# Performance work log

Hardware: AMD Instinct MI355X
Metric: run time of the kernel (lower is better)

The kernel has to match this reference:

```python
import jax, jax.numpy as jnp
import numpy as np

L, B, T, D, H, M = 2, 4, 1024, 256, 4, 1024
EPS = 1e-5  # hk.LayerNorm default


def setup_inputs() -> dict:
    key = jax.random.key(0)
    ks = jax.random.split(key, 12)
    s_in = (2.0 / D) ** 0.5       # VarianceScaling(2.0), fan_in = D
    s_o = (2.0 / (H * D)) ** 0.5  # fan_in = H*D for final projection
    s_m = (1.0 / M) ** 0.5
    g = lambda k, shape, s: jax.random.normal(k, shape, jnp.float32) * s
    return {
        "queries": g(ks[0], (B, T, D), 1.0),
        "Wq": g(ks[1], (L, D, H * D), s_in),
        "bq": jnp.zeros((L, H * D), jnp.float32),
        "Wk": g(ks[2], (L, D, H * D), s_in),
        "bk": jnp.zeros((L, H * D), jnp.float32),
        "Wv": g(ks[3], (L, D, H * D), s_in),
        "bv": jnp.zeros((L, H * D), jnp.float32),
        "Wo": g(ks[4], (L, H * D, D), s_o),
        "bo": jnp.zeros((L, D), jnp.float32),
        "ln1_s": jnp.ones((L, D), jnp.float32),
        "ln1_b": jnp.zeros((L, D), jnp.float32),
        "W1": g(ks[5], (L, D, M), s_in),
        "b1": jnp.zeros((L, M), jnp.float32),
        "W2": g(ks[6], (L, M, D), s_m),
        "b2": jnp.zeros((L, D), jnp.float32),
        "ln2_s": jnp.ones((L, D), jnp.float32),
        "ln2_b": jnp.zeros((L, D), jnp.float32),
    }


def _layernorm(x, s, o):
    m = jnp.mean(x, axis=-1, keepdims=True)
    v = jnp.var(x, axis=-1, keepdims=True)
    return (x - m) * jax.lax.rsqrt(v + EPS) * s + o


def _block(x, Wq, bq, Wk, bk, Wv, bv, Wo, bo, ln1_s, ln1_b, W1, b1, W2, b2, ln2_s, ln2_b):
    # Multi-head self-attention with per-head dim = D (key_size == qkv_size)
    q = (x @ Wq + bq).reshape(B, T, H, D)
    k = (x @ Wk + bk).reshape(B, T, H, D)
    v = (x @ Wv + bv).reshape(B, T, H, D)
    q = q / jnp.sqrt(jnp.float32(D))
    attn = jnp.einsum('bqhd,bkhd->bhqk', q, k)   # [B,H,T,T]
    attn = jax.nn.softmax(attn, axis=-1)
    o = jnp.einsum('bhqk,bkhd->bqhd', attn, v).reshape(B, T, H * D)
    o = o @ Wo + bo
    # post-norm residual 1
    x = _layernorm(o + x, ln1_s, ln1_b)
    # MLP: Linear(D->M) + ReLU + Linear(M->D)
    h = jax.nn.relu(x @ W1 + b1)
    m = h @ W2 + b2
    return _layernorm(m + x, ln2_s, ln2_b)


def reference(queries, Wq, bq, Wk, bk, Wv, bv, Wo, bo, ln1_s, ln1_b,
              W1, b1, W2, b2, ln2_s, ln2_b):
    x = queries
    for i in range(L):
        x = _block(x, Wq[i], bq[i], Wk[i], bk[i], Wv[i], bv[i], Wo[i], bo[i],
                   ln1_s[i], ln1_b[i], W1[i], b1[i], W2[i], b2[i],
                   ln2_s[i], ln2_b[i])
    return x
```

## Files before the change

### kernel.cpp

```cpp
#include <hip/hip_runtime.h>
#include <hip/hip_bf16.h>

#define CL 2
#define CB 4
#define CT 1024
#define CD 256
#define CH 4
#define CM 1024
#define CHD (CH * CD)
#define NROW (CB * CT)

typedef unsigned short ushort_t;
typedef __attribute__((ext_vector_type(8))) short short8v;
typedef __attribute__((ext_vector_type(4))) float float4v;

#define LOG2E 1.44269504088896f

__device__ __forceinline__ float bf2f(unsigned short u) {
    return __uint_as_float(((unsigned int)u) << 16);
}
__device__ __forceinline__ unsigned short f2bf(float f) {
    unsigned int x = __float_as_uint(f);
    return (unsigned short)((x + 0x7fffu + ((x >> 16) & 1u)) >> 16);
}

__global__ __launch_bounds__(256) void detect_kernel(
    const ushort_t* __restrict__ w, int n, int* __restrict__ flag)
{
    __shared__ int red[256];
    int c = 0;
    for (int i = threadIdx.x; i < n; i += 256) {
        float v = bf2f(w[i]);
        if (!(fabsf(v) <= 1e6f)) c++;
    }
    red[threadIdx.x] = c;
    __syncthreads();
    for (int s = 128; s > 0; s >>= 1) {
        if (threadIdx.x < s) red[threadIdx.x] += red[threadIdx.x + s];
        __syncthreads();
    }
    if (threadIdx.x == 0) flag[0] = (red[0] < 8) ? 1 : 0;
}

__global__ __launch_bounds__(256) void tconv_kernel(
    const void* __restrict__ in, ushort_t* __restrict__ out,
    int R, int C, long inzs, long outzs, long ioff,
    const int* __restrict__ flagp)
{
    const int fbf = *flagp;
    __shared__ float tile[32][33];
    const long zi = ioff + (long)blockIdx.z * inzs;
    const long zo = (long)blockIdx.z * outzs;
    const int r0 = blockIdx.y * 32;
    const int c0 = blockIdx.x * 32;
    const int tx = threadIdx.x & 31;
    const int ty = threadIdx.x >> 5;
#pragma unroll
    for (int i = 0; i < 32; i += 8) {
        const long idx = zi + (long)(r0 + ty + i) * C + c0 + tx;
        tile[ty + i][tx] = fbf ? bf2f(((const ushort_t*)in)[idx])
                               : ((const float*)in)[idx];
    }
    __syncthreads();
#pragma unroll
    for (int i = 0; i < 32; i += 8)
        out[zo + (long)(c0 + ty + i) * R + r0 + tx] = f2bf(tile[tx][ty + i]);
}

__global__ __launch_bounds__(256) void qkv_proj(
    const ushort_t* __restrict__ A, const ushort_t* __restrict__ B,
    const void* __restrict__ bq, const void* __restrict__ bk,
    const void* __restrict__ bv, ushort_t* __restrict__ qk,
    ushort_t* __restrict__ vT, long boff, const int* __restrict__ flagp)
{
    const long m0 = (long)blockIdx.y * 128;
    const long n0 = (long)blockIdx.x * 128;

    __shared__ __align__(16) ushort_t As[128 * 32];
    __shared__ __align__(16) ushort_t Bs[128 * 32];

    const int tid = threadIdx.x;
    const int wave = tid >> 6;
    const int lane = tid & 63;
    const int quad = lane >> 4;
    const int lrow = lane & 15;
    const int wm = (wave >> 1) * 64;
    const int wn = (wave & 1) * 64;

    float4v acc[4][4];
#pragma unroll
    for (int i = 0; i < 4; ++i)
#pragma unroll
        for (int j = 0; j < 4; ++j)
            acc[i][j] = (float4v){0.f, 0.f, 0.f, 0.f};

    for (int k0 = 0; k0 < 256; k0 += 32) {
        __syncthreads();
#pragma unroll
        for (int p = 0; p < 2; ++p) {
            const int c = p * 256 + tid;
            const int row = c >> 2;
            const int kk = (c & 3) << 3;
            *reinterpret_cast<short8v*>(&As[c << 3]) =
                *reinterpret_cast<const short8v*>(&A[(m0 + row) * 256 + k0 + kk]);
            *reinterpret_cast<short8v*>(&Bs[c << 3]) =
                *reinterpret_cast<const short8v*>(&B[(n0 + row) * 256 + k0 + kk]);
        }
        __syncthreads();

        short8v af[4], bfv[4];
#pragma unroll
        for (int i = 0; i < 4; ++i) {
            af[i]  = *reinterpret_cast<const short8v*>(&As[(wm + i * 16 + lrow) * 32 + quad * 8]);
            bfv[i] = *reinterpret_cast<const short8v*>(&Bs[(wn + i * 16 + lrow) * 32 + quad * 8]);
        }
#pragma unroll
        for (int mi = 0; mi < 4; ++mi)
#pragma unroll
            for (int ni = 0; ni < 4; ++ni)
                acc[mi][ni] = __builtin_amdgcn_mfma_f32_16x16x32_bf16(
                    af[mi], bfv[ni], acc[mi][ni], 0, 0, 0);
    }

    const int fbf = *flagp;
#pragma unroll
    for (int mi = 0; mi < 4; ++mi) {
#pragma unroll
        for (int ni = 0; ni < 4; ++ni) {
            const long col = n0 + wn + ni * 16 + lrow;
            const long row0 = m0 + wm + mi * 16 + quad * 4;
            const void* bp;
            long bn;
            if (col < 1024)      { bp = bq; bn = col; }
            else if (col < 2048) { bp = bk; bn = col - 1024; }
            else                 { bp = bv; bn = col - 2048; }
            const float bias = fbf ? bf2f(((const ushort_t*)bp)[boff + bn])
                                   : ((const float*)bp)[boff + bn];
            if (col < 2048) {
#pragma unroll
                for (int r = 0; r < 4; ++r)
                    qk[(row0 + r) * 2048 + col] = f2bf(acc[mi][ni][r] + bias);
            } else {
                const long d = col - 2048;
                const long addr = ((row0 >> 10) << 2) * 262144 + d * 1024 + (row0 & 1023);
                ushort4 u;
                u.x = f2bf(acc[mi][ni][0] + bias);
                u.y = f2bf(acc[mi][ni][1] + bias);
                u.z = f2bf(acc[mi][ni][2] + bias);
                u.w = f2bf(acc[mi][ni][3] + bias);
                *reinterpret_cast<ushort4*>(&vT[addr]) = u;
            }
        }
    }
}

template <int AMODE>
__global__ __launch_bounds__(256) void mgemm64s(
    const ushort_t* __restrict__ A, const ushort_t* __restrict__ Ap1,
    const float2* __restrict__ ml, const ushort_t* __restrict__ B,
    float* __restrict__ P, int K2, int lda, int ldb)
{
    const int z = blockIdx.z;
    const long m0 = (long)blockIdx.y * 64;
    const long n0 = (long)blockIdx.x * 64;
    const int k_beg = z * K2;

    __shared__ __align__(16) ushort_t As[64 * 32];
    __shared__ __align__(16) ushort_t Bs[64 * 32];

    const int tid = threadIdx.x;
    const int wave = tid >> 6;
    const int lane = tid & 63;
    const int quad = lane >> 4;
    const int lrow = lane & 15;
    const int wm = (wave >> 1) * 32;
    const int wn = (wave & 1) * 32;

    const int ar = tid >> 2;
    const int ak = (tid & 3) << 3;

    float4v acc[2][2];
#pragma unroll
    for (int i = 0; i < 2; ++i)
#pragma unroll
        for (int j = 0; j < 2; ++j)
            acc[i][j] = (float4v){0.f, 0.f, 0.f, 0.f};

    for (int k0 = k_beg; k0 < k_beg + K2; k0 += 32) {
        __syncthreads();
        if constexpr (AMODE == 0) {
            *reinterpret_cast<short8v*>(&As[tid << 3]) =
                *reinterpret_cast<const short8v*>(&A[(m0 + ar) * (long)lda + k0 + ak]);
        } else {
            const long m = m0 + ar;
            const int hh = (k0 + ak) >> 8;
            const int bh = ((int)(m >> 10) << 2) + hh;
            const int trow = (int)(m & 1023);
            const float2 v0 = ml[bh * 1024 + trow];
            const float2 v1 = ml[(16 + bh) * 1024 + trow];
            const float mm = fmaxf(v0.x, v1.x);
            const float a0 = exp2f(v0.x - mm);
            const float a1 = exp2f(v1.x - mm);
            const float inv = 1.0f / (v0.y * a0 + v1.y * a1);
            const ushort4 u0a = *reinterpret_cast<const ushort4*>(&A[m * 1024 + k0 + ak]);
            const ushort4 u0b = *reinterpret_cast<const ushort4*>(&A[m * 1024 + k0 + ak + 4]);
            const ushort4 u1a = *reinterpret_cast<const ushort4*>(&Ap1[m * 1024 + k0 + ak]);
            const ushort4 u1b = *reinterpret_cast<const ushort4*>(&Ap1[m * 1024 + k0 + ak + 4]);
            short8v t8;
            t8[0] = (short)f2bf((bf2f(u0a.x) * a0 + bf2f(u1a.x) * a1) * inv);
            t8[1] = (short)f2bf((bf2f(u0a.y) * a0 + bf2f(u1a.y) * a1) * inv);
            t8[2] = (short)f2bf((bf2f(u0a.z) * a0 + bf2f(u1a.z) * a1) * inv);
            t8[3] = (short)f2bf((bf2f(u0a.w) * a0 + bf2f(u1a.w) * a1) * inv);
            t8[4] = (short)f2bf((bf2f(u0b.x) * a0 + bf2f(u1b.x) * a1) * inv);
            t8[5] = (short)f2bf((bf2f(u0b.y) * a0 + bf2f(u1b.y) * a1) * inv);
            t8[6] = (short)f2bf((bf2f(u0b.z) * a0 + bf2f(u1b.z) * a1) * inv);
            t8[7] = (short)f2bf((bf2f(u0b.w) * a0 + bf2f(u1b.w) * a1) * inv);
            *reinterpret_cast<short8v*>(&As[tid << 3]) = t8;
        }
        *reinterpret_cast<short8v*>(&Bs[tid << 3]) =
            *reinterpret_cast<const short8v*>(&B[(n0 + ar) * (long)ldb + k0 + ak]);
        __syncthreads();

        short8v af[2], bfv[2];
#pragma unroll
        for (int i = 0; i < 2; ++i) {
            af[i]  = *reinterpret_cast<const short8v*>(&As[(wm + i * 16 + lrow) * 32 + quad * 8]);
            bfv[i] = *reinterpret_cast<const short8v*>(&Bs[(wn + i * 16 + lrow) * 32 + quad * 8]);
        }
#pragma unroll
        for (int mi = 0; mi < 2; ++mi)
#pragma unroll
            for (int ni = 0; ni < 2; ++ni)
                acc[mi][ni] = __builtin_amdgcn_mfma_f32_16x16x32_bf16(
                    af[mi], bfv[ni], acc[mi][ni], 0, 0, 0);
    }

    float* Pz = P + (long)z * NROW * CD;
#pragma unroll
    for (int mi = 0; mi < 2; ++mi)
#pragma unroll
        for (int ni = 0; ni < 2; ++ni) {
            const long col = n0 + wn + ni * 16 + lrow;
            const long row0 = m0 + wm + mi * 16 + quad * 4;
#pragma unroll
            for (int r = 0; r < 4; ++r)
                Pz[(row0 + r) * CD + col] = acc[mi][ni][r];
        }
}

template <int RELU>
__global__ __launch_bounds__(256) void mgemm64b(
    const ushort_t* __restrict__ A, const ushort_t* __restrict__ B,
    const void* __restrict__ bias, ushort_t* __restrict__ C,
    int K, int lda, int ldb, int ldc, long boff,
    const int* __restrict__ flagp)
{
    const long m0 = (long)blockIdx.y * 64;
    const long n0 = (long)blockIdx.x * 64;

    __shared__ __align__(16) ushort_t As[64 * 32];
    __shared__ __align__(16) ushort_t Bs[64 * 32];

    const int tid = threadIdx.x;
    const int wave = tid >> 6;
    const int lane = tid & 63;
    const int quad = lane >> 4;
    const int lrow = lane & 15;
    const int wm = (wave >> 1) * 32;
    const int wn = (wave & 1) * 32;

    const int ar = tid >> 2;
    const int ak = (tid & 3) << 3;

    float4v acc[2][2];
#pragma unroll
    for (int i = 0; i < 2; ++i)
#pragma unroll
        for (int j = 0; j < 2; ++j)
            acc[i][j] = (float4v){0.f, 0.f, 0.f, 0.f};

    for (int k0 = 0; k0 < K; k0 += 32) {
        __syncthreads();
        *reinterpret_cast<short8v*>(&As[tid << 3]) =
            *reinterpret_cast<const short8v*>(&A[(m0 + ar) * (long)lda + k0 + ak]);
        *reinterpret_cast<short8v*>(&Bs[tid << 3]) =
            *reinterpret_cast<const short8v*>(&B[(n0 + ar) * (long)ldb + k0 + ak]);
        __syncthreads();

        short8v af[2], bfv[2];
#pragma unroll
        for (int i = 0; i < 2; ++i) {
            af[i]  = *reinterpret_cast<const short8v*>(&As[(wm + i * 16 + lrow) * 32 + quad * 8]);
            bfv[i] = *reinterpret_cast<const short8v*>(&Bs[(wn + i * 16 + lrow) * 32 + quad * 8]);
        }
#pragma unroll
        for (int mi = 0; mi < 2; ++mi)
#pragma unroll
            for (int ni = 0; ni < 2; ++ni)
                acc[mi][ni] = __builtin_amdgcn_mfma_f32_16x16x32_bf16(
                    af[mi], bfv[ni], acc[mi][ni], 0, 0, 0);
    }

    const int fbf = *flagp;
#pragma unroll
    for (int mi = 0; mi < 2; ++mi)
#pragma unroll
        for (int ni = 0; ni < 2; ++ni) {
            const long col = n0 + wn + ni * 16 + lrow;
            const long row0 = m0 + wm + mi * 16 + quad * 4;
            const float bv = fbf ? bf2f(((const ushort_t*)bias)[boff + col])
                                 : ((const float*)bias)[boff + col];
#pragma unroll
            for (int r = 0; r < 4; ++r) {
                float v = acc[mi][ni][r] + bv;
                if (RELU) v = fmaxf(v, 0.f);
                C[(row0 + r) * (long)ldc + col] = f2bf(v);
            }
        }
}

__global__ __launch_bounds__(256) void flash_attn(
    const ushort_t* __restrict__ qk, const ushort_t* __restrict__ vT,
    ushort_t* __restrict__ op0, ushort_t* __restrict__ op1,
    float2* __restrict__ ml)
{
    const int bx = blockIdx.x;
    const int bh = bx & 15;
    const int qt = (bx >> 4) & 15;
    const int ck = bx >> 8;
    const int b = bh >> 2, h = bh & 3;

    __shared__ __align__(16) ushort_t Ks[32 * 264];
    __shared__ __align__(16) ushort_t Vs[256 * 40];
    __shared__ __align__(16) ushort_t Ps[4][16 * 40];

    const int tid = threadIdx.x;
    const int wave = tid >> 6;
    const int lane = tid & 63;
    const int quad = lane >> 4;
    const int lrow = lane & 15;

    const long qrow0 = (long)b * CT + qt * 64;
    const int qcol = h * 256;
    const int kcol = 1024 + h * 256;
    const long vbase = (long)bh * 256 * 1024;
    const float SC = 0.0625f * LOG2E;

    short8v qf[8];
#pragma unroll
    for (int kk = 0; kk < 8; ++kk)
        qf[kk] = *reinterpret_cast<const short8v*>(
            &qk[(qrow0 + wave * 16 + lrow) * 2048 + qcol + kk * 32 + quad * 8]);

    float m4[4], l4[4];
#pragma unroll
    for (int r = 0; r < 4; ++r) { m4[r] = -1e30f; l4[r] = 0.f; }
    float4v oacc[16];
#pragma unroll
    for (int i = 0; i < 16; ++i) oacc[i] = (float4v){0.f, 0.f, 0.f, 0.f};

    const int t_beg = ck * 512;
    for (int t0 = t_beg; t0 < t_beg + 512; t0 += 32) {
        __syncthreads();
#pragma unroll
        for (int p = 0; p < 4; ++p) {
            const int c = p * 256 + tid;
            {
                const int r = c >> 5, col = (c & 31) * 8;
                *reinterpret_cast<short8v*>(&Ks[r * 264 + col]) =
                    *reinterpret_cast<const short8v*>(
                        &qk[((long)b * CT + t0 + r) * 2048 + kcol + col]);
            }
            {
                const int r = c >> 2, col = (c & 3) * 8;
                *reinterpret_cast<short8v*>(&Vs[r * 40 + col]) =
                    *reinterpret_cast<const short8v*>(
                        &vT[vbase + (long)r * 1024 + t0 + col]);
            }
        }
        __syncthreads();

        float4v sacc[2];
        sacc[0] = (float4v){0.f, 0.f, 0.f, 0.f};
        sacc[1] = (float4v){0.f, 0.f, 0.f, 0.f};
#pragma unroll
        for (int kk = 0; kk < 8; ++kk) {
#pragma unroll
            for (int ni = 0; ni < 2; ++ni) {
                short8v bk = *reinterpret_cast<const short8v*>(
                    &Ks[(ni * 16 + lrow) * 264 + kk * 32 + quad * 8]);
                sacc[ni] = __builtin_amdgcn_mfma_f32_16x16x32_bf16(
                    qf[kk], bk, sacc[ni], 0, 0, 0);
            }
        }
#pragma unroll
        for (int ni = 0; ni < 2; ++ni)
#pragma unroll
            for (int r = 0; r < 4; ++r)
                sacc[ni][r] *= SC;

        float alpha4[4];
#pragma unroll
        for (int r = 0; r < 4; ++r) {
            float mx = fmaxf(sacc[0][r], sacc[1][r]);
#pragma unroll
            for (int sh = 1; sh < 16; sh <<= 1)
                mx = fmaxf(mx, __shfl_xor(mx, sh));
            const float mnew = fmaxf(m4[r], mx);
            alpha4[r] = exp2f(m4[r] - mnew);
            m4[r] = mnew;
        }
#pragma unroll
        for (int ni = 0; ni < 2; ++ni)
#pragma unroll
            for (int r = 0; r < 4; ++r) {
                const float pv = exp2f(sacc[ni][r] - m4[r]);
                sacc[ni][r] = pv;
                Ps[wave][(quad * 4 + r) * 40 + ni * 16 + lrow] = f2bf(pv);
            }
#pragma unroll
        for (int r = 0; r < 4; ++r) {
            float s = sacc[0][r] + sacc[1][r];
#pragma unroll
            for (int sh = 1; sh < 16; sh <<= 1)
                s += __shfl_xor(s, sh);
            l4[r] = l4[r] * alpha4[r] + s;
        }
        const float amin = fminf(fminf(alpha4[0], alpha4[1]),
                                 fminf(alpha4[2], alpha4[3]));
        if (__ballot(amin < 1.0f) != 0ull) {
#pragma unroll
            for (int ni = 0; ni < 16; ++ni)
#pragma unroll
                for (int r = 0; r < 4; ++r)
                    oacc[ni][r] *= alpha4[r];
        }

        {
            short8v ap = *reinterpret_cast<const short8v*>(
                &Ps[wave][lrow * 40 + quad * 8]);
#pragma unroll
            for (int ni = 0; ni < 16; ++ni) {
                short8v bv = *reinterpret_cast<const short8v*>(
                    &Vs[(ni * 16 + lrow) * 40 + quad * 8]);
                oacc[ni] = __builtin_amdgcn_mfma_f32_16x16x32_bf16(
                    ap, bv, oacc[ni], 0, 0, 0);
            }
        }
    }

#pragma unroll
    for (int r = 0; r < 4; ++r)
        if (lrow == 0)
            ml[((ck << 4) + bh) * 1024 + qt * 64 + wave * 16 + quad * 4 + r] =
                make_float2(m4[r], l4[r]);

    ushort_t* op = ck ? op1 : op0;
#pragma unroll
    for (int ni = 0; ni < 16; ++ni)
#pragma unroll
        for (int r = 0; r < 4; ++r)
            op[(qrow0 + wave * 16 + quad * 4 + r) * 1024 + (h << 8) + ni * 16 + lrow]
                = f2bf(oacc[ni][r]);
}

template <int FINAL>
__global__ __launch_bounds__(256) void ln_p(
    const float* __restrict__ p, const void* __restrict__ gb, long gboff,
    const ushort_t* __restrict__ res, const void* __restrict__ sc,
    const void* __restrict__ bi, void* __restrict__ out, long loff,
    const int* __restrict__ flagp)
{
    const int fbf = *flagp;
    const long row = (long)blockIdx.x * CD;
    const int t = threadIdx.x;
    const float gbv = fbf ? bf2f(((const ushort_t*)gb)[gboff + t])
                          : ((const float*)gb)[gboff + t];
    const float x = p[row + t] + p[(long)NROW * CD + row + t] + gbv + bf2f(res[row + t]);

    __shared__ float r1[256];
    __shared__ float r2[256];
    r1[t] = x;
    r2[t] = x * x;
    __syncthreads();
    for (int s = 128; s > 0; s >>= 1) {
        if (t < s) { r1[t] += r1[t + s]; r2[t] += r2[t + s]; }
        __syncthreads();
    }
    const float mean = r1[0] * (1.0f / CD);
    const float var = r2[0] * (1.0f / CD) - mean * mean;
    const float rstd = rsqrtf(var + 1e-5f);
    const float s_v = fbf ? bf2f(((const ushort_t*)sc)[loff + t]) : ((const float*)sc)[loff + t];
    const float b_v = fbf ? bf2f(((const ushort_t*)bi)[loff + t]) : ((const float*)bi)[loff + t];
    const float y = (x - mean) * rstd * s_v + b_v;
    if constexpr (FINAL) {
        if (fbf) ((ushort_t*)out)[row + t] = f2bf(y);
        else     ((float*)out)[row + t] = y;
    } else {
        ((ushort_t*)out)[row + t] = f2bf(y);
    }
}

__global__ __launch_bounds__(256) void in_convert(
    const void* __restrict__ in, ushort_t* __restrict__ x,
    const int* __restrict__ flagp)
{
    const int fbf = *flagp;
    const long i = ((long)blockIdx.x * 256 + threadIdx.x) << 2;
    if (fbf) {
        *reinterpret_cast<ushort4*>(x + i) =
            *reinterpret_cast<const ushort4*>((const ushort_t*)in + i);
    } else {
        float4 f = *reinterpret_cast<const float4*>((const float*)in + i);
        ushort4 u;
        u.x = f2bf(f.x); u.y = f2bf(f.y); u.z = f2bf(f.z); u.w = f2bf(f.w);
        *reinterpret_cast<ushort4*>(x + i) = u;
    }
}

extern "C" void kernel_launch(void* const* d_in, const int* in_sizes, int n_in,
                              void* d_out, int out_size, void* d_ws, size_t ws_size,
                              hipStream_t stream)
{
    const void* queries = d_in[0];
    const void* Wq = d_in[1];  const void* bq = d_in[2];
    const void* Wk = d_in[3];  const void* bk = d_in[4];
    const void* Wv = d_in[5];  const void* bv = d_in[6];
    const void* Wo = d_in[7];  const void* bo = d_in[8];
    const void* ln1s = d_in[9];  const void* ln1b = d_in[10];
    const void* W1 = d_in[11]; const void* b1 = d_in[12];
    const void* W2 = d_in[13]; const void* b2 = d_in[14];
    const void* ln2s = d_in[15]; const void* ln2b = d_in[16];

    char* p = (char*)d_ws;
    int* flagp = (int*)p;             p += 256;
    ushort_t* wqkvT = (ushort_t*)p;   p += (long)CL * 3072 * 256 * 2;
    ushort_t* w1T   = (ushort_t*)p;   p += (long)CL * 1024 * 256 * 2;
    ushort_t* wscr  = (ushort_t*)p;   p += (long)256 * 1024 * 2;
    ushort_t* xa    = (ushort_t*)p;   p += (long)NROW * CD * 2;
    ushort_t* qk    = (ushort_t*)p;   p += (long)NROW * 2048 * 2;
    ushort_t* vT    = (ushort_t*)p;   p += (long)16 * 256 * 1024 * 2;
    ushort_t* op0   = (ushort_t*)p;   p += (long)NROW * 1024 * 2;
    ushort_t* op1   = (ushort_t*)p;   p += (long)NROW * 1024 * 2;
    float2*   ml    = (float2*)p;     p += (long)2 * 16 * 1024 * 8;
    ushort_t* h     = vT;
    float*    pgem  = (float*)qk;

    detect_kernel<<<1, 256, 0, stream>>>((const ushort_t*)Wq, 2048, flagp);

    tconv_kernel<<<dim3(32, 8, CL), 256, 0, stream>>>(
        Wq, wqkvT, 256, 1024, 256 * 1024, 3072 * 256, 0, flagp);
    tconv_kernel<<<dim3(32, 8, CL), 256, 0, stream>>>(
        Wk, wqkvT + 1024 * 256, 256, 1024, 256 * 1024, 3072 * 256, 0, flagp);
    tconv_kernel<<<dim3(32, 8, CL), 256, 0, stream>>>(
        Wv, wqkvT + 2048 * 256, 256, 1024, 256 * 1024, 3072 * 256, 0, flagp);
    tconv_kernel<<<dim3(32, 8, CL), 256, 0, stream>>>(
        W1, w1T, 256, 1024, 256 * 1024, 1024 * 256, 0, flagp);

    in_convert<<<(NROW * CD) / 1024, 256, 0, stream>>>(queries, xa, flagp);

    for (int l = 0; l < CL; ++l) {
        qkv_proj<<<dim3(24, 32, 1), 256, 0, stream>>>(
            xa, wqkvT + (long)l * 3072 * 256, bq, bk, bv, qk, vT,
            (long)l * 1024, flagp);
        tconv_kernel<<<dim3(8, 32, 1), 256, 0, stream>>>(
            Wo, wscr, 1024, 256, 0, 0, (long)l * 1024 * 256, flagp);
        flash_attn<<<512, 256, 0, stream>>>(qk, vT, op0, op1, ml);
        mgemm64s<1><<<dim3(4, 64, 2), 256, 0, stream>>>(
            op0, op1, ml, wscr, pgem, 512, 1024, 1024);
        ln_p<0><<<NROW, 256, 0, stream>>>(pgem, bo, (long)l * 256, xa,
                                          ln1s, ln1b, xa, (long)l * 256, flagp);
        mgemm64b<1><<<dim3(16, 64, 1), 256, 0, stream>>>(
            xa, w1T + (long)l * 1024 * 256, b1, h,
            256, 256, 256, 1024, (long)l * 1024, flagp);
        tconv_kernel<<<dim3(8, 32, 1), 256, 0, stream>>>(
            W2, wscr, 1024, 256, 0, 0, (long)l * 1024 * 256, flagp);
        mgemm64s<0><<<dim3(4, 64, 2), 256, 0, stream>>>(
            h, nullptr, nullptr, wscr, pgem, 512, 1024, 1024);
        if (l == CL - 1)
            ln_p<1><<<NROW, 256, 0, stream>>>(pgem, b2, (long)l * 256, xa,
                                              ln2s, ln2b, d_out, (long)l * 256, flagp);
        else
            ln_p<0><<<NROW, 256, 0, stream>>>(pgem, b2, (long)l * 256, xa,
                                              ln2s, ln2b, xa, (long)l * 256, flagp);
    }
}
```

Before: 348.0 us.

## Swap QK MFMA operands for row-per-lane softmax and merge weight transpose launches

The QK^T MFMA operands are swapped, so each lane holds scores for a single query row. The online-softmax max and sum then need only two cross-quad shuffles instead of four-step reductions over four rows, and the P tile is written to LDS in the transposed layout. Per-row alpha values are gathered with shuffles only when a rescale is needed. Separately, the four initial weight-transpose launches are merged into one kernel, and the per-layer Wo and W2 transposes are merged into one launch writing a doubled scratch buffer, cutting the number of kernel launches.

```diff
diff --git a/kernel.cpp b/kernel.cpp
--- a/kernel.cpp
+++ b/kernel.cpp
@@ -42,29 +42,63 @@
     if (threadIdx.x == 0) flag[0] = (red[0] < 8) ? 1 : 0;
 }
 
-__global__ __launch_bounds__(256) void tconv_kernel(
-    const void* __restrict__ in, ushort_t* __restrict__ out,
-    int R, int C, long inzs, long outzs, long ioff,
+__global__ __launch_bounds__(256) void tconv_all(
+    const void* __restrict__ Wq, const void* __restrict__ Wk,
+    const void* __restrict__ Wv, const void* __restrict__ W1,
+    ushort_t* __restrict__ wqkvT, ushort_t* __restrict__ w1T,
     const int* __restrict__ flagp)
 {
     const int fbf = *flagp;
+    const int z = blockIdx.z;
+    const int which = z >> 1, l = z & 1;
+    const void* in = (which == 0) ? Wq : (which == 1) ? Wk
+                   : (which == 2) ? Wv : W1;
+    ushort_t* out = (which < 3)
+        ? wqkvT + (long)l * 3072 * 256 + (long)which * 1024 * 256
+        : w1T + (long)l * 1024 * 256;
+    const long zi = (long)l * 262144;
+
     __shared__ float tile[32][33];
-    const long zi = ioff + (long)blockIdx.z * inzs;
-    const long zo = (long)blockIdx.z * outzs;
     const int r0 = blockIdx.y * 32;
     const int c0 = blockIdx.x * 32;
     const int tx = threadIdx.x & 31;
     const int ty = threadIdx.x >> 5;
 #pragma unroll
     for (int i = 0; i < 32; i += 8) {
-        const long idx = zi + (long)(r0 + ty + i) * C + c0 + tx;
+        const long idx = zi + (long)(r0 + ty + i) * 1024 + c0 + tx;
         tile[ty + i][tx] = fbf ? bf2f(((const ushort_t*)in)[idx])
                                : ((const float*)in)[idx];
     }
     __syncthreads();
 #pragma unroll
     for (int i = 0; i < 32; i += 8)
-        out[zo + (long)(c0 + ty + i) * R + r0 + tx] = f2bf(tile[tx][ty + i]);
+        out[(long)(c0 + ty + i) * 256 + r0 + tx] = f2bf(tile[tx][ty + i]);
+}
+
+__global__ __launch_bounds__(256) void tconv2(
+    const void* __restrict__ Wo, const void* __restrict__ W2,
+    ushort_t* __restrict__ wscr, long ioff, const int* __restrict__ flagp)
+{
+    const int fbf = *flagp;
+    const int z = blockIdx.z;
+    const void* in = z ? W2 : Wo;
+    ushort_t* out = wscr + (long)z * 262144;
+
+    __shared__ float tile[32][33];
+    const int r0 = blockIdx.y * 32;
+    const int c0 = blockIdx.x * 32;
+    const int tx = threadIdx.x & 31;
+    const int ty = threadIdx.x >> 5;
+#pragma unroll
+    for (int i = 0; i < 32; i += 8) {
+        const long idx = ioff + (long)(r0 + ty + i) * 256 + c0 + tx;
+        tile[ty + i][tx] = fbf ? bf2f(((const ushort_t*)in)[idx])
+                               : ((const float*)in)[idx];
+    }
+    __syncthreads();
+#pragma unroll
+    for (int i = 0; i < 32; i += 8)
+        out[(long)(c0 + ty + i) * 1024 + r0 + tx] = f2bf(tile[tx][ty + i]);
 }
 
 __global__ __launch_bounds__(256) void qkv_proj(
@@ -352,9 +386,7 @@
         qf[kk] = *reinterpret_cast<const short8v*>(
             &qk[(qrow0 + wave * 16 + lrow) * 2048 + qcol + kk * 32 + quad * 8]);
 
-    float m4[4], l4[4];
-#pragma unroll
-    for (int r = 0; r < 4; ++r) { m4[r] = -1e30f; l4[r] = 0.f; }
+    float mrun = -1e30f, lrun = 0.f;
     float4v oacc[16];
 #pragma unroll
     for (int i = 0; i < 16; ++i) oacc[i] = (float4v){0.f, 0.f, 0.f, 0.f};
@@ -390,7 +422,7 @@
                 short8v bk = *reinterpret_cast<const short8v*>(
                     &Ks[(ni * 16 + lrow) * 264 + kk * 32 + quad * 8]);
                 sacc[ni] = __builtin_amdgcn_mfma_f32_16x16x32_bf16(
-                    qf[kk], bk, sacc[ni], 0, 0, 0);
+                    bk, qf[kk], sacc[ni], 0, 0, 0);
             }
         }
 #pragma unroll
@@ -399,41 +431,39 @@
             for (int r = 0; r < 4; ++r)
                 sacc[ni][r] *= SC;
 
-        float alpha4[4];
-#pragma unroll
-        for (int r = 0; r < 4; ++r) {
-            float mx = fmaxf(sacc[0][r], sacc[1][r]);
-#pragma unroll
-            for (int sh = 1; sh < 16; sh <<= 1)
-                mx = fmaxf(mx, __shfl_xor(mx, sh));
-            const float mnew = fmaxf(m4[r], mx);
-            alpha4[r] = exp2f(m4[r] - mnew);
-            m4[r] = mnew;
-        }
+        float mx = fmaxf(fmaxf(fmaxf(sacc[0][0], sacc[0][1]),
+                               fmaxf(sacc[0][2], sacc[0][3])),
+                         fmaxf(fmaxf(sacc[1][0], sacc[1][1]),
+                               fmaxf(sacc[1][2], sacc[1][3])));
+        mx = fmaxf(mx, __shfl_xor(mx, 16));
+        mx = fmaxf(mx, __shfl_xor(mx, 32));
+        const float mnew = fmaxf(mrun, mx);
+        const float alpha = exp2f(mrun - mnew);
+        mrun = mnew;
+
+        float s = 0.f;
 #pragma unroll
         for (int ni = 0; ni < 2; ++ni)
 #pragma unroll
             for (int r = 0; r < 4; ++r) {
-                const float pv = exp2f(sacc[ni][r] - m4[r]);
-                sacc[ni][r] = pv;
-                Ps[wave][(quad * 4 + r) * 40 + ni * 16 + lrow] = f2bf(pv);
+                const float pv = exp2f(sacc[ni][r] - mnew);
+                s += pv;
+                Ps[wave][lrow * 40 + ni * 16 + quad * 4 + r] = f2bf(pv);
             }
-#pragma unroll
-        for (int r = 0; r < 4; ++r) {
-            float s = sacc[0][r] + sacc[1][r];
-#pragma unroll
-            for (int sh = 1; sh < 16; sh <<= 1)
-                s += __shfl_xor(s, sh);
-            l4[r] = l4[r] * alpha4[r] + s;
-        }
-        const float amin = fminf(fminf(alpha4[0], alpha4[1]),
-                                 fminf(alpha4[2], alpha4[3]));
-        if (__ballot(amin < 1.0f) != 0ull) {
+        s += __shfl_xor(s, 16);
+        s += __shfl_xor(s, 32);
+        lrun = lrun * alpha + s;
+
+        if (__ballot(alpha < 1.0f) != 0ull) {
+            float a4[4];
+#pragma unroll
+            for (int r = 0; r < 4; ++r)
+                a4[r] = __shfl(alpha, quad * 4 + r);
 #pragma unroll
             for (int ni = 0; ni < 16; ++ni)
 #pragma unroll
                 for (int r = 0; r < 4; ++r)
-                    oacc[ni][r] *= alpha4[r];
+                    oacc[ni][r] *= a4[r];
         }
 
         {
@@ -449,11 +479,9 @@
         }
     }
 
-#pragma unroll
-    for (int r = 0; r < 4; ++r)
-        if (lrow == 0)
-            ml[((ck << 4) + bh) * 1024 + qt * 64 + wave * 16 + quad * 4 + r] =
-                make_float2(m4[r], l4[r]);
+    if (quad == 0)
+        ml[((ck << 4) + bh) * 1024 + qt * 64 + wave * 16 + lrow] =
+            make_float2(mrun, lrun);
 
     ushort_t* op = ck ? op1 : op0;
 #pragma unroll
@@ -536,7 +564,7 @@
     int* flagp = (int*)p;             p += 256;
     ushort_t* wqkvT = (ushort_t*)p;   p += (long)CL * 3072 * 256 * 2;
     ushort_t* w1T   = (ushort_t*)p;   p += (long)CL * 1024 * 256 * 2;
-    ushort_t* wscr  = (ushort_t*)p;   p += (long)256 * 1024 * 2;
+    ushort_t* wscr  = (ushort_t*)p;   p += (long)2 * 256 * 1024 * 2;
     ushort_t* xa    = (ushort_t*)p;   p += (long)NROW * CD * 2;
     ushort_t* qk    = (ushort_t*)p;   p += (long)NROW * 2048 * 2;
     ushort_t* vT    = (ushort_t*)p;   p += (long)16 * 256 * 1024 * 2;
@@ -548,14 +576,8 @@
 
     detect_kernel<<<1, 256, 0, stream>>>((const ushort_t*)Wq, 2048, flagp);
 
-    tconv_kernel<<<dim3(32, 8, CL), 256, 0, stream>>>(
-        Wq, wqkvT, 256, 1024, 256 * 1024, 3072 * 256, 0, flagp);
-    tconv_kernel<<<dim3(32, 8, CL), 256, 0, stream>>>(
-        Wk, wqkvT + 1024 * 256, 256, 1024, 256 * 1024, 3072 * 256, 0, flagp);
-    tconv_kernel<<<dim3(32, 8, CL), 256, 0, stream>>>(
-        Wv, wqkvT + 2048 * 256, 256, 1024, 256 * 1024, 3072 * 256, 0, flagp);
-    tconv_kernel<<<dim3(32, 8, CL), 256, 0, stream>>>(
-        W1, w1T, 256, 1024, 256 * 1024, 1024 * 256, 0, flagp);
+    tconv_all<<<dim3(32, 8, 8), 256, 0, stream>>>(
+        Wq, Wk, Wv, W1, wqkvT, w1T, flagp);
 
     in_convert<<<(NROW * CD) / 1024, 256, 0, stream>>>(queries, xa, flagp);
 
@@ -563,8 +585,8 @@
         qkv_proj<<<dim3(24, 32, 1), 256, 0, stream>>>(
             xa, wqkvT + (long)l * 3072 * 256, bq, bk, bv, qk, vT,
             (long)l * 1024, flagp);
-        tconv_kernel<<<dim3(8, 32, 1), 256, 0, stream>>>(
-            Wo, wscr, 1024, 256, 0, 0, (long)l * 1024 * 256, flagp);
+        tconv2<<<dim3(8, 32, 2), 256, 0, stream>>>(
+            Wo, W2, wscr, (long)l * 1024 * 256, flagp);
         flash_attn<<<512, 256, 0, stream>>>(qk, vT, op0, op1, ml);
         mgemm64s<1><<<dim3(4, 64, 2), 256, 0, stream>>>(
             op0, op1, ml, wscr, pgem, 512, 1024, 1024);
@@ -573,10 +595,8 @@
         mgemm64b<1><<<dim3(16, 64, 1), 256, 0, stream>>>(
             xa, w1T + (long)l * 1024 * 256, b1, h,
             256, 256, 256, 1024, (long)l * 1024, flagp);
-        tconv_kernel<<<dim3(8, 32, 1), 256, 0, stream>>>(
-            W2, wscr, 1024, 256, 0, 0, (long)l * 1024 * 256, flagp);
         mgemm64s<0><<<dim3(4, 64, 2), 256, 0, stream>>>(
-            h, nullptr, nullptr, wscr, pgem, 512, 1024, 1024);
+            h, nullptr, nullptr, wscr + 262144, pgem, 512, 1024, 1024);
         if (l == CL - 1)
             ln_p<1><<<NROW, 256, 0, stream>>>(pgem, b2, (long)l * 256, xa,
                                               ln2s, ln2b, d_out, (long)l * 256, flagp);
```

Result: faster. 316.9 us (-8.9%).
